# Kernel optimization log

Hardware: AMD Instinct MI355X
Metric: run time of the kernel (lower is better)

Reference implementation:

```python
import jax, jax.numpy as jnp
import numpy as np

W_SIM, W_REC, W_FREQ, W_IMP, W_TYPE = 0.45, 0.2, 0.15, 0.1, 0.1
TYPE_WEIGHT = 0.9
DECAY_HALF_LIFE = 200.0
TEMPERATURE = 0.07
LN_EPS = 1e-5


def _l2norm(v, axis=-1):
    # matches torch F.normalize (eps=1e-12 clamp on the norm)
    n = jnp.linalg.norm(v, axis=axis, keepdims=True)
    return v / jnp.maximum(n, 1e-12)


def setup_inputs() -> dict:
    key = jax.random.key(0)
    ks = jax.random.split(key, 8)
    B, D, S = 16384, 2048, 64
    s = 1.0 / np.sqrt(D)
    x = jax.random.normal(ks[0], (B, D), jnp.float32)
    prototypes = _l2norm(jax.random.normal(ks[1], (S, D), jnp.float32))
    proto_conf = jax.random.uniform(ks[2], (S,), jnp.float32)
    proto_age = jax.random.uniform(ks[3], (S,), jnp.float32)
    proto_evidence = jnp.ones((S,), jnp.float32)
    W_in = jax.random.normal(ks[4], (D, D), jnp.float32) * s
    b_in = jnp.zeros((D,), jnp.float32)
    Wr1 = jax.random.normal(ks[5], (D // 2, D), jnp.float32) * s
    br1 = jnp.zeros((D // 2,), jnp.float32)
    Wr2 = jax.random.normal(ks[6], (4, D // 2), jnp.float32) * (1.0 / np.sqrt(D // 2))
    br2 = jnp.zeros((4,), jnp.float32)
    W_out = jax.random.normal(ks[7], (D, 2 * D), jnp.float32) * (1.0 / np.sqrt(2 * D))
    b_out = jnp.zeros((D,), jnp.float32)
    ln_w = jnp.ones((D,), jnp.float32)
    ln_b = jnp.zeros((D,), jnp.float32)
    return {"x": x, "prototypes": prototypes, "proto_conf": proto_conf,
            "proto_age": proto_age, "proto_evidence": proto_evidence,
            "W_in": W_in, "b_in": b_in, "Wr1": Wr1, "br1": br1,
            "Wr2": Wr2, "br2": br2, "W_out": W_out, "b_out": b_out,
            "ln_w": ln_w, "ln_b": ln_b}


def reference(x, prototypes, proto_conf, proto_age, proto_evidence,
              W_in, b_in, Wr1, br1, Wr2, br2, W_out, b_out, ln_w, ln_b):
    S = prototypes.shape[0]
    protos_per_type = S // 4

    # in_proj + normalize
    h = x @ W_in.T + b_in                                  # [B, D]
    h_norm = _l2norm(h)

    # type router: Linear -> GELU(exact) -> Linear -> softmax
    r = jax.nn.gelu(x @ Wr1.T + br1, approximate=False)    # [B, D/2]
    type_weights = jax.nn.softmax(r @ Wr2.T + br2, axis=-1)  # [B, 4]

    # prototype similarity
    p_norm = _l2norm(prototypes)
    raw_sim = h_norm @ p_norm.T                            # [B, S]

    type_assign = jnp.arange(S) // protos_per_type         # [S] in {0..3}
    type_mask = type_weights[:, type_assign]               # [B, S]
    weighted_sim = raw_sim * type_mask * proto_conf[None, :]

    # multi-factor salience (fused elementwise)
    recency = jnp.exp(-proto_age / DECAY_HALF_LIFE)[None, :]
    freq_norm = (jnp.log(proto_evidence + 1.0) /
                 (jnp.log(proto_evidence.max() + 2.0) + 1e-8))[None, :]
    sal = (W_SIM * weighted_sim + W_REC * recency + W_FREQ * freq_norm
           + W_IMP * proto_conf[None, :] + W_TYPE * TYPE_WEIGHT)
    sal = jnp.clip(sal, 0.0, 1.0)

    # attention over prototype bank
    attn = jax.nn.softmax(sal / TEMPERATURE, axis=-1)       # [B, S]
    retrieved = attn @ prototypes                           # [B, D]

    combined = jnp.concatenate([x, retrieved], axis=-1)     # [B, 2D]
    out = jax.nn.gelu(combined @ W_out.T + b_out, approximate=False)
    # dropout is identity in eval mode

    # residual + LayerNorm (biased variance, eps=1e-5)
    y = out + x
    mu = jnp.mean(y, axis=-1, keepdims=True)
    var = jnp.mean((y - mu) ** 2, axis=-1, keepdims=True)
    return ln_w * (y - mu) / jnp.sqrt(var + LN_EPS) + ln_b
```

## Files before the change

### kernel.cpp

```cpp
#include <hip/hip_runtime.h>
#include <hip/hip_bf16.h>
#include <cstdint>

#define DEV __device__ __forceinline__

typedef __bf16 bf16x8 __attribute__((ext_vector_type(8)));
typedef float f32x4 __attribute__((ext_vector_type(4)));
typedef unsigned short ushort_t;
typedef ushort_t ushort8 __attribute__((ext_vector_type(8)));

DEV ushort_t f2bf(float f) {
  union { float f; uint32_t u; } x; x.f = f;
  uint32_t r = (x.u + 0x7fffu + ((x.u >> 16) & 1u)) >> 16;
  return (ushort_t)r;
}
DEV float bf2f(ushort_t b) {
  union { uint32_t u; float f; } x; x.u = ((uint32_t)b) << 16;
  return x.f;
}
DEV float gelu_exact(float v) {
  return 0.5f * v * (1.0f + erff(v * 0.70710678118654752f));
}
DEV void gload_lds16(const void* g, void* l) {
  __builtin_amdgcn_global_load_lds(
      (const __attribute__((address_space(1))) void*)g,
      (__attribute__((address_space(3))) void*)l, 16, 0, 0);
}


__global__ __launch_bounds__(64) void prep_scal(
    const float* __restrict__ conf, const float* __restrict__ age,
    const float* __restrict__ ev, float* __restrict__ base, float* __restrict__ cs) {
  int l = threadIdx.x;
  float e = ev[l];
  float m = e;
  #pragma unroll
  for (int d = 1; d < 64; d <<= 1) m = fmaxf(m, __shfl_xor(m, d));
  float freq = logf(e + 1.f) / (logf(m + 2.f) + 1e-8f);
  base[l] = 0.2f * expf(-age[l] * (1.f / 200.f)) + 0.15f * freq + 0.1f * conf[l] + 0.09f;
  cs[l] = 0.45f * conf[l];
}

__global__ __launch_bounds__(256) void prep_pnorm(
    const float* __restrict__ protos, const float* __restrict__ b_in,
    float* __restrict__ p_norm, float* __restrict__ dvec) {
  const int s = blockIdx.x, t = threadIdx.x;
  const float* p = protos + (size_t)s * 2048;
  float vals[8];
  float ss = 0.f, sb = 0.f;
  #pragma unroll
  for (int ii = 0; ii < 2; ++ii) {
    float4 v = *(const float4*)(p + t * 8 + ii * 4);
    float4 bi = *(const float4*)(b_in + t * 8 + ii * 4);
    vals[ii * 4 + 0] = v.x; vals[ii * 4 + 1] = v.y; vals[ii * 4 + 2] = v.z; vals[ii * 4 + 3] = v.w;
    ss += v.x * v.x + v.y * v.y + v.z * v.z + v.w * v.w;
    sb += v.x * bi.x + v.y * bi.y + v.z * bi.z + v.w * bi.w;
  }
  #pragma unroll
  for (int d = 1; d < 64; d <<= 1) { ss += __shfl_xor(ss, d); sb += __shfl_xor(sb, d); }
  __shared__ float red[8];
  if ((t & 63) == 0) { red[t >> 6] = ss; red[4 + (t >> 6)] = sb; }
  __syncthreads();
  ss = red[0] + red[1] + red[2] + red[3];
  sb = red[4] + red[5] + red[6] + red[7];
  float inv = 1.f / fmaxf(sqrtf(ss), 1e-12f);
  #pragma unroll
  for (int k = 0; k < 8; ++k) p_norm[(size_t)s * 2048 + t * 8 + k] = vals[k] * inv;
  if (t == 0) dvec[s] = sb * inv;
}


__global__ __launch_bounds__(256) void conv_x(const float* __restrict__ x, ushort_t* __restrict__ xa) {
  size_t e = ((size_t)blockIdx.x * 256 + threadIdx.x) * 8;
  int row = (int)(e >> 11), col = (int)(e & 2047);
  float4 f0 = *(const float4*)(x + e);
  float4 f1 = *(const float4*)(x + e + 4);
  ushort8 o;
  o[0] = f2bf(f0.x); o[1] = f2bf(f0.y); o[2] = f2bf(f0.z); o[3] = f2bf(f0.w);
  o[4] = f2bf(f1.x); o[5] = f2bf(f1.y); o[6] = f2bf(f1.z); o[7] = f2bf(f1.w);
  *(ushort8*)(xa + (size_t)row * 2112 + col) = o;
}

__global__ __launch_bounds__(256) void conv_wbig(const float* __restrict__ W_in,
                                                 const float* __restrict__ Wr1,
                                                 ushort_t* __restrict__ wbig) {
  size_t e = ((size_t)blockIdx.x * 256 + threadIdx.x) * 8;
  int row = (int)(e >> 11), col = (int)(e & 2047);
  if (row >= 3072 && row < 3136) return;
  ushort8 o;
  if (row < 3072) {
    const float* src = (row < 2048) ? (W_in + (size_t)row * 2048 + col)
                                    : (Wr1 + (size_t)(row - 2048) * 2048 + col);
    float4 f0 = *(const float4*)(src);
    float4 f1 = *(const float4*)(src + 4);
    o[0] = f2bf(f0.x); o[1] = f2bf(f0.y); o[2] = f2bf(f0.z); o[3] = f2bf(f0.w);
    o[4] = f2bf(f1.x); o[5] = f2bf(f1.y); o[6] = f2bf(f1.z); o[7] = f2bf(f1.w);
  } else {
    o = ushort8{0, 0, 0, 0, 0, 0, 0, 0};
  }
  *(ushort8*)(wbig + (size_t)row * 2048 + col) = o;
}

__global__ __launch_bounds__(256) void conv_ww(const float* __restrict__ W_out,
                                               ushort_t* __restrict__ wwm) {
  size_t e = ((size_t)blockIdx.x * 256 + threadIdx.x) * 8;
  int n = (int)(e >> 11), c = (int)(e & 2047);
  float4 f0 = *(const float4*)(W_out + (size_t)n * 4096 + c);
  float4 f1 = *(const float4*)(W_out + (size_t)n * 4096 + c + 4);
  ushort8 o;
  o[0] = f2bf(f0.x); o[1] = f2bf(f0.y); o[2] = f2bf(f0.z); o[3] = f2bf(f0.w);
  o[4] = f2bf(f1.x); o[5] = f2bf(f1.y); o[6] = f2bf(f1.z); o[7] = f2bf(f1.w);
  *(ushort8*)(wwm + (size_t)n * 2112 + c) = o;
}

__global__ __launch_bounds__(256) void small_p2(const float* __restrict__ p_norm,
                                                const float* __restrict__ W_in,
                                                ushort_t* __restrict__ wbig) {
  __shared__ float pn[8][128];
  const int t = threadIdx.x;
  const int k = blockIdx.x * 128 + (t & 127);
  const int sh = t >> 7;
  const int s0 = blockIdx.y * 8;
  float acc[4] = {0.f, 0.f, 0.f, 0.f};
  for (int j0 = 0; j0 < 2048; j0 += 128) {
    __syncthreads();
    {
      int sl = t >> 5;
      int j4 = (t & 31) * 4;
      *(float4*)&pn[sl][j4] = *(const float4*)&p_norm[(size_t)(s0 + sl) * 2048 + j0 + j4];
    }
    __syncthreads();
    #pragma unroll 8
    for (int jj = 0; jj < 128; ++jj) {
      float wv = W_in[(size_t)(j0 + jj) * 2048 + k];
      #pragma unroll
      for (int i = 0; i < 4; ++i) acc[i] += pn[sh * 4 + i][jj] * wv;
    }
  }
  #pragma unroll
  for (int i = 0; i < 4; ++i)
    wbig[(size_t)(3072 + s0 + sh * 4 + i) * 2048 + k] = f2bf(acc[i]);
}

__global__ __launch_bounds__(256) void small_R(const float* __restrict__ protos,
                                               const float* __restrict__ W_out,
                                               ushort_t* __restrict__ wwm) {
  __shared__ float pch[64][68];
  __shared__ float wch[16][68];
  const int t = threadIdx.x;
  const int n_loc = t >> 4;
  const int sb = t & 15;
  const int n0 = blockIdx.x * 16;
  float acc[4] = {0.f, 0.f, 0.f, 0.f};
  for (int k0 = 0; k0 < 2048; k0 += 64) {
    __syncthreads();
    #pragma unroll
    for (int ii = 0; ii < 4; ++ii) {
      int lin4 = t * 4 + ii;
      int s = lin4 >> 4;
      int k4 = (lin4 & 15) * 4;
      *(float4*)&pch[s][k4] = *(const float4*)&protos[(size_t)s * 2048 + k0 + k4];
    }
    {
      int n_l = t >> 4;
      int k4 = (t & 15) * 4;
      *(float4*)&wch[n_l][k4] = *(const float4*)&W_out[(size_t)(n0 + n_l) * 4096 + 2048 + k0 + k4];
    }
    __syncthreads();
    #pragma unroll 8
    for (int kk = 0; kk < 64; ++kk) {
      float wv = wch[n_loc][kk];
      #pragma unroll
      for (int i = 0; i < 4; ++i) acc[i] += pch[sb + 16 * i][kk] * wv;
    }
  }
  #pragma unroll
  for (int i = 0; i < 4; ++i)
    wwm[(size_t)(n0 + n_loc) * 2112 + 2048 + sb + 16 * i] = f2bf(acc[i]);
}

__global__ __launch_bounds__(256, 4) void gemm_head(
    const ushort_t* __restrict__ A, const ushort_t* __restrict__ Bw,
    const float* __restrict__ bias0, const float* __restrict__ bias1,
    float* __restrict__ rn2part, ushort_t* __restrict__ out1, float* __restrict__ out2) {
  __shared__ ushort_t As[128 * 32];
  __shared__ ushort_t Bs[128 * 32];
  const int tid = threadIdx.x;
  const int w = tid >> 6, l = tid & 63;
  const int bm = blockIdx.x * 128;
  const int bn = blockIdx.y * 128;
  const int srow = tid >> 2;
  const int scol = (tid & 3) * 8;
  const int wm = (w >> 1) * 64, wn = (w & 1) * 64;
  const int lr = l & 15, lk = (l >> 4) * 8;

  f32x4 acc[4][4];
  #pragma unroll
  for (int i = 0; i < 4; ++i)
    #pragma unroll
    for (int j = 0; j < 4; ++j) acc[i][j] = f32x4{0.f, 0.f, 0.f, 0.f};

  for (int k0 = 0; k0 < 2048; k0 += 32) {
    __syncthreads();
    #pragma unroll
    for (int r = 0; r < 2; ++r) {
      int row = srow + r * 64;
      gload_lds16(A + (size_t)(bm + row) * 2112 + k0 + scol,
                  (char*)As + (size_t)(r * 256 + tid) * 16);
    }
    #pragma unroll
    for (int r = 0; r < 2; ++r) {
      int row = srow + r * 64;
      gload_lds16(Bw + (size_t)(bn + row) * 2048 + k0 + scol,
                  (char*)Bs + (size_t)(r * 256 + tid) * 16);
    }
    __syncthreads();
    bf16x8 af[4], bf_[4];
    #pragma unroll
    for (int i = 0; i < 4; ++i) af[i] = *(const bf16x8*)&As[(wm + i * 16 + lr) * 32 + lk];
    #pragma unroll
    for (int j = 0; j < 4; ++j) bf_[j] = *(const bf16x8*)&Bs[(wn + j * 16 + lr) * 32 + lk];
    #pragma unroll
    for (int i = 0; i < 4; ++i)
      #pragma unroll
      for (int j = 0; j < 4; ++j)
        acc[i][j] = __builtin_amdgcn_mfma_f32_16x16x32_bf16(af[i], bf_[j], acc[i][j], 0, 0, 0);
  }

  const int lg = l >> 4;
  #pragma unroll
  for (int i = 0; i < 4; ++i) {
    #pragma unroll
    for (int q = 0; q < 4; ++q) {
      const int grow = bm + wm + i * 16 + lg * 4 + q;
      float ss = 0.f;
      #pragma unroll
      for (int j = 0; j < 4; ++j) {
        const int gcol = bn + wn + j * 16 + lr;
        float v = acc[i][j][q];
        if (gcol < 2048) {
          v += bias0[gcol];
          ss += v * v;
        } else if (gcol < 3072) {
          v += bias1[gcol - 2048];
          out1[(size_t)grow * 1024 + (gcol - 2048)] = f2bf(gelu_exact(v));
        } else if (gcol < 3136) {
          out2[(size_t)grow * 64 + (gcol - 3072)] = v;
        }
      }
      if (bn < 2048) {
        ss += __shfl_xor(ss, 1);
        ss += __shfl_xor(ss, 2);
        ss += __shfl_xor(ss, 4);
        ss += __shfl_xor(ss, 8);
        if (lr == 0) rn2part[(size_t)grow * 16 + blockIdx.y] = ss;
      }
    }
  }
}

__global__ __launch_bounds__(256, 4) void gemm_out(
    const ushort_t* __restrict__ A, const ushort_t* __restrict__ Bw,
    const float* __restrict__ bias0, float* __restrict__ out0) {
  __shared__ ushort_t As[128 * 32];
  __shared__ ushort_t Bs[128 * 32];
  const int tid = threadIdx.x;
  const int w = tid >> 6, l = tid & 63;
  const int bm = blockIdx.x * 128;
  const int bn = blockIdx.y * 128;
  const int srow = tid >> 2;
  const int scol = (tid & 3) * 8;
  const int wm = (w >> 1) * 64, wn = (w & 1) * 64;
  const int lr = l & 15, lk = (l >> 4) * 8;

  f32x4 acc[4][4];
  #pragma unroll
  for (int i = 0; i < 4; ++i)
    #pragma unroll
    for (int j = 0; j < 4; ++j) acc[i][j] = f32x4{0.f, 0.f, 0.f, 0.f};

  for (int k0 = 0; k0 < 2112; k0 += 32) {
    __syncthreads();
    #pragma unroll
    for (int r = 0; r < 2; ++r) {
      int row = srow + r * 64;
      gload_lds16(A + (size_t)(bm + row) * 2112 + k0 + scol,
                  (char*)As + (size_t)(r * 256 + tid) * 16);
    }
    #pragma unroll
    for (int r = 0; r < 2; ++r) {
      int row = srow + r * 64;
      gload_lds16(Bw + (size_t)(bn + row) * 2112 + k0 + scol,
                  (char*)Bs + (size_t)(r * 256 + tid) * 16);
    }
    __syncthreads();
    bf16x8 af[4], bf_[4];
    #pragma unroll
    for (int i = 0; i < 4; ++i) af[i] = *(const bf16x8*)&As[(wm + i * 16 + lr) * 32 + lk];
    #pragma unroll
    for (int j = 0; j < 4; ++j) bf_[j] = *(const bf16x8*)&Bs[(wn + j * 16 + lr) * 32 + lk];
    #pragma unroll
    for (int i = 0; i < 4; ++i)
      #pragma unroll
      for (int j = 0; j < 4; ++j)
        acc[i][j] = __builtin_amdgcn_mfma_f32_16x16x32_bf16(af[i], bf_[j], acc[i][j], 0, 0, 0);
  }

  const int lg = l >> 4;
  #pragma unroll
  for (int i = 0; i < 4; ++i)
    #pragma unroll
    for (int j = 0; j < 4; ++j)
      #pragma unroll
      for (int q = 0; q < 4; ++q) {
        const int grow = bm + wm + i * 16 + lg * 4 + q;
        const int gcol = bn + wn + j * 16 + lr;
        float v = acc[i][j][q] + bias0[gcol];
        float g = gelu_exact(v);
        out0[(size_t)grow * 2048 + gcol] = g + bf2f(A[(size_t)grow * 2112 + gcol]);
      }
}

__global__ __launch_bounds__(256) void attn_k(
    const ushort_t* __restrict__ r_bf, const float* __restrict__ Wr2,
    const float* __restrict__ br2, const float* __restrict__ rn2p,
    const float* __restrict__ rproj, const float* __restrict__ dvec,
    const float* __restrict__ base, const float* __restrict__ cs,
    ushort_t* __restrict__ xa) {
  const int b = blockIdx.x * 4 + (threadIdx.x >> 6);
  const int l = threadIdx.x & 63;
  const ushort_t* rrow = r_bf + (size_t)b * 1024;
  float t0 = 0.f, t1 = 0.f, t2 = 0.f, t3 = 0.f;
  #pragma unroll
  for (int m = 0; m < 16; ++m) {
    int k = l + m * 64;
    float rv = bf2f(rrow[k]);
    t0 += rv * Wr2[k];
    t1 += rv * Wr2[1024 + k];
    t2 += rv * Wr2[2048 + k];
    t3 += rv * Wr2[3072 + k];
  }
  #pragma unroll
  for (int d = 1; d < 64; d <<= 1) {
    t0 += __shfl_xor(t0, d); t1 += __shfl_xor(t1, d);
    t2 += __shfl_xor(t2, d); t3 += __shfl_xor(t3, d);
  }
  t0 += br2[0]; t1 += br2[1]; t2 += br2[2]; t3 += br2[3];
  float mx = fmaxf(fmaxf(t0, t1), fmaxf(t2, t3));
  float e0 = expf(t0 - mx), e1 = expf(t1 - mx), e2 = expf(t2 - mx), e3 = expf(t3 - mx);
  float sinv = 1.f / (e0 + e1 + e2 + e3);
  float tw0 = e0 * sinv, tw1 = e1 * sinv, tw2 = e2 * sinv, tw3 = e3 * sinv;
  const int ty = l >> 4;
  float twv = (ty == 0) ? tw0 : ((ty == 1) ? tw1 : ((ty == 2) ? tw2 : tw3));

  float rsum = 0.f;
  #pragma unroll
  for (int t = 0; t < 16; ++t) rsum += rn2p[(size_t)b * 16 + t];
  float inv = 1.f / fmaxf(sqrtf(rsum), 1e-12f);
  float rp = rproj[(size_t)b * 64 + l] + dvec[l];
  float sal = cs[l] * twv * (rp * inv) + base[l];
  sal = fminf(fmaxf(sal, 0.f), 1.f);
  float logit = sal * (1.f / 0.07f);
  float lm = logit;
  #pragma unroll
  for (int d = 1; d < 64; d <<= 1) lm = fmaxf(lm, __shfl_xor(lm, d));
  float ex = expf(logit - lm);
  float es = ex;
  #pragma unroll
  for (int d = 1; d < 64; d <<= 1) es += __shfl_xor(es, d);
  float attn = ex / es;
  xa[(size_t)b * 2112 + 2048 + l] = f2bf(attn);
}

__global__ __launch_bounds__(256) void ln_k(float* __restrict__ y,
                                            const float* __restrict__ lw,
                                            const float* __restrict__ lb) {
  const int b = blockIdx.x, t = threadIdx.x;
  float* row = y + (size_t)b * 2048;
  float4 v0 = *(const float4*)(row + t * 8);
  float4 v1 = *(const float4*)(row + t * 8 + 4);
  float s = v0.x + v0.y + v0.z + v0.w + v1.x + v1.y + v1.z + v1.w;
  float s2 = v0.x * v0.x + v0.y * v0.y + v0.z * v0.z + v0.w * v0.w +
             v1.x * v1.x + v1.y * v1.y + v1.z * v1.z + v1.w * v1.w;
  #pragma unroll
  for (int d = 1; d < 64; d <<= 1) { s += __shfl_xor(s, d); s2 += __shfl_xor(s2, d); }
  __shared__ float red[8];
  if ((t & 63) == 0) { red[t >> 6] = s; red[4 + (t >> 6)] = s2; }
  __syncthreads();
  float ts = red[0] + red[1] + red[2] + red[3];
  float ts2 = red[4] + red[5] + red[6] + red[7];
  const float mu = ts * (1.f / 2048.f);
  const float inv = 1.f / sqrtf(ts2 * (1.f / 2048.f) - mu * mu + 1e-5f);
  float4 w0 = *(const float4*)(lw + t * 8), w1 = *(const float4*)(lw + t * 8 + 4);
  float4 b0 = *(const float4*)(lb + t * 8), b1 = *(const float4*)(lb + t * 8 + 4);
  float4 o0, o1;
  o0.x = (v0.x - mu) * inv * w0.x + b0.x;
  o0.y = (v0.y - mu) * inv * w0.y + b0.y;
  o0.z = (v0.z - mu) * inv * w0.z + b0.z;
  o0.w = (v0.w - mu) * inv * w0.w + b0.w;
  o1.x = (v1.x - mu) * inv * w1.x + b1.x;
  o1.y = (v1.y - mu) * inv * w1.y + b1.y;
  o1.z = (v1.z - mu) * inv * w1.z + b1.z;
  o1.w = (v1.w - mu) * inv * w1.w + b1.w;
  *(float4*)(row + t * 8) = o0;
  *(float4*)(row + t * 8 + 4) = o1;
}

extern "C" void kernel_launch(void* const* d_in, const int* in_sizes, int n_in,
                              void* d_out, int out_size, void* d_ws, size_t ws_size,
                              hipStream_t stream) {
  const float* x      = (const float*)d_in[0];
  const float* protos = (const float*)d_in[1];
  const float* conf   = (const float*)d_in[2];
  const float* age    = (const float*)d_in[3];
  const float* ev     = (const float*)d_in[4];
  const float* W_in   = (const float*)d_in[5];
  const float* b_in   = (const float*)d_in[6];
  const float* Wr1    = (const float*)d_in[7];
  const float* br1    = (const float*)d_in[8];
  const float* Wr2    = (const float*)d_in[9];
  const float* br2    = (const float*)d_in[10];
  const float* W_out  = (const float*)d_in[11];
  const float* b_out  = (const float*)d_in[12];
  const float* ln_w   = (const float*)d_in[13];
  const float* ln_b   = (const float*)d_in[14];
  float* out = (float*)d_out;

  char* ws = (char*)d_ws;
  size_t off = 0;
  auto take = [&](size_t bytes) {
    char* p = ws + off;
    off = (off + bytes + 255) & ~(size_t)255;
    return p;
  };
  ushort_t* xa     = (ushort_t*)take((size_t)16384 * 2112 * 2);
  ushort_t* wbig   = (ushort_t*)take((size_t)3200 * 2048 * 2);
  ushort_t* wwm    = (ushort_t*)take((size_t)2048 * 2112 * 2);
  ushort_t* rbf    = (ushort_t*)take((size_t)16384 * 1024 * 2);
  float*    rproj  = (float*)take((size_t)16384 * 64 * 4);
  float*    rn2p   = (float*)take((size_t)16384 * 16 * 4);
  float*    pnorm  = (float*)take((size_t)64 * 2048 * 4);
  float*    base   = (float*)take(256);
  float*    cs     = (float*)take(256);
  float*    dvec   = (float*)take(256);
  (void)in_sizes; (void)n_in; (void)out_size; (void)ws_size;

  prep_scal<<<1, 64, 0, stream>>>(conf, age, ev, base, cs);
  prep_pnorm<<<64, 256, 0, stream>>>(protos, b_in, pnorm, dvec);
  conv_x<<<16384, 256, 0, stream>>>(x, xa);
  conv_wbig<<<3200, 256, 0, stream>>>(W_in, Wr1, wbig);
  conv_ww<<<2048, 256, 0, stream>>>(W_out, wwm);
  small_p2<<<dim3(16, 8), 256, 0, stream>>>(pnorm, W_in, wbig);
  small_R<<<128, 256, 0, stream>>>(protos, W_out, wwm);
  gemm_head<<<dim3(128, 25), 256, 0, stream>>>(xa, wbig, b_in, br1, rn2p, rbf, rproj);
  attn_k<<<4096, 256, 0, stream>>>(rbf, Wr2, br2, rn2p, rproj, dvec, base, cs, xa);
  gemm_out<<<dim3(128, 16), 256, 0, stream>>>(xa, wwm, b_out, out);
  ln_k<<<16384, 256, 0, stream>>>(out, ln_w, ln_b);
}
```

Before: 829.4 us.

## Enlarge GEMM block tiles to 256x128 with 512-thread blocks

Both main bf16 MFMA GEMMs (head and output projection) now use 512-thread blocks covering 256 rows instead of 128, with the grid halved along M. Each block loads two A row slabs and one B slab per k-step, so every B tile staged in LDS feeds twice as many output rows. The aim is to cut global and LDS traffic for the weight operand per FLOP. The risk is the launch bound of (512, 4): it asks for more resident waves per SIMD, which may force the 64-float accumulator array into a tight register budget and cause spills, and the larger blocks lower the block count available for scheduling.

```diff
diff --git a/kernel.cpp b/kernel.cpp
--- a/kernel.cpp
+++ b/kernel.cpp
@@ -179,15 +179,15 @@
     wwm[(size_t)(n0 + n_loc) * 2112 + 2048 + sb + 16 * i] = f2bf(acc[i]);
 }
 
-__global__ __launch_bounds__(256, 4) void gemm_head(
+__global__ __launch_bounds__(512, 4) void gemm_head(
     const ushort_t* __restrict__ A, const ushort_t* __restrict__ Bw,
     const float* __restrict__ bias0, const float* __restrict__ bias1,
     float* __restrict__ rn2part, ushort_t* __restrict__ out1, float* __restrict__ out2) {
-  __shared__ ushort_t As[128 * 32];
+  __shared__ ushort_t As[256 * 32];
   __shared__ ushort_t Bs[128 * 32];
   const int tid = threadIdx.x;
   const int w = tid >> 6, l = tid & 63;
-  const int bm = blockIdx.x * 128;
+  const int bm = blockIdx.x * 256;
   const int bn = blockIdx.y * 128;
   const int srow = tid >> 2;
   const int scol = (tid & 3) * 8;
@@ -202,18 +202,12 @@
 
   for (int k0 = 0; k0 < 2048; k0 += 32) {
     __syncthreads();
-    #pragma unroll
-    for (int r = 0; r < 2; ++r) {
-      int row = srow + r * 64;
-      gload_lds16(A + (size_t)(bm + row) * 2112 + k0 + scol,
-                  (char*)As + (size_t)(r * 256 + tid) * 16);
-    }
-    #pragma unroll
-    for (int r = 0; r < 2; ++r) {
-      int row = srow + r * 64;
-      gload_lds16(Bw + (size_t)(bn + row) * 2048 + k0 + scol,
-                  (char*)Bs + (size_t)(r * 256 + tid) * 16);
-    }
+    gload_lds16(A + (size_t)(bm + srow) * 2112 + k0 + scol,
+                (char*)As + (size_t)tid * 16);
+    gload_lds16(A + (size_t)(bm + 128 + srow) * 2112 + k0 + scol,
+                (char*)As + (size_t)(512 + tid) * 16);
+    gload_lds16(Bw + (size_t)(bn + srow) * 2048 + k0 + scol,
+                (char*)Bs + (size_t)tid * 16);
     __syncthreads();
     bf16x8 af[4], bf_[4];
     #pragma unroll
@@ -259,14 +253,14 @@
   }
 }
 
-__global__ __launch_bounds__(256, 4) void gemm_out(
+__global__ __launch_bounds__(512, 4) void gemm_out(
     const ushort_t* __restrict__ A, const ushort_t* __restrict__ Bw,
     const float* __restrict__ bias0, float* __restrict__ out0) {
-  __shared__ ushort_t As[128 * 32];
+  __shared__ ushort_t As[256 * 32];
   __shared__ ushort_t Bs[128 * 32];
   const int tid = threadIdx.x;
   const int w = tid >> 6, l = tid & 63;
-  const int bm = blockIdx.x * 128;
+  const int bm = blockIdx.x * 256;
   const int bn = blockIdx.y * 128;
   const int srow = tid >> 2;
   const int scol = (tid & 3) * 8;
@@ -281,18 +275,12 @@
 
   for (int k0 = 0; k0 < 2112; k0 += 32) {
     __syncthreads();
-    #pragma unroll
-    for (int r = 0; r < 2; ++r) {
-      int row = srow + r * 64;
-      gload_lds16(A + (size_t)(bm + row) * 2112 + k0 + scol,
-                  (char*)As + (size_t)(r * 256 + tid) * 16);
-    }
-    #pragma unroll
-    for (int r = 0; r < 2; ++r) {
-      int row = srow + r * 64;
-      gload_lds16(Bw + (size_t)(bn + row) * 2112 + k0 + scol,
-                  (char*)Bs + (size_t)(r * 256 + tid) * 16);
-    }
+    gload_lds16(A + (size_t)(bm + srow) * 2112 + k0 + scol,
+                (char*)As + (size_t)tid * 16);
+    gload_lds16(A + (size_t)(bm + 128 + srow) * 2112 + k0 + scol,
+                (char*)As + (size_t)(512 + tid) * 16);
+    gload_lds16(Bw + (size_t)(bn + srow) * 2112 + k0 + scol,
+                (char*)Bs + (size_t)tid * 16);
     __syncthreads();
     bf16x8 af[4], bf_[4];
     #pragma unroll
@@ -452,8 +440,8 @@
   conv_ww<<<2048, 256, 0, stream>>>(W_out, wwm);
   small_p2<<<dim3(16, 8), 256, 0, stream>>>(pnorm, W_in, wbig);
   small_R<<<128, 256, 0, stream>>>(protos, W_out, wwm);
-  gemm_head<<<dim3(128, 25), 256, 0, stream>>>(xa, wbig, b_in, br1, rn2p, rbf, rproj);
+  gemm_head<<<dim3(64, 25), 512, 0, stream>>>(xa, wbig, b_in, br1, rn2p, rbf, rproj);
   attn_k<<<4096, 256, 0, stream>>>(rbf, Wr2, br2, rn2p, rproj, dvec, base, cs, xa);
-  gemm_out<<<dim3(128, 16), 256, 0, stream>>>(xa, wwm, b_out, out);
+  gemm_out<<<dim3(64, 16), 512, 0, stream>>>(xa, wwm, b_out, out);
   ln_k<<<16384, 256, 0, stream>>>(out, ln_w, ln_b);
 }
```

New measurement: 825.6 us. About the same (-0.5%).
